# Kernel optimization log

Measured on AMD Instinct MI355X. Metric: run time of the kernel, lower is better.

Reference implementation:

```python
import jax, jax.numpy as jnp
import numpy as np

B, D, H, NB = 4096, 2048, 2048, 4
BIN, BOUT = D // NB, H // NB
EPS = 1e-5


def _block_linear(x, W, b):
    # x: [B, nb*bin], W: [nb, bin, bout], b: [nb, bout] -> [B, nb*bout]
    xr = x.reshape(x.shape[0], NB, BIN)
    y = jnp.einsum('bni,nio->bno', xr, W) + b
    return y.reshape(x.shape[0], NB * BOUT)


def setup_inputs() -> dict:
    key = jax.random.key(0)
    ks = jax.random.split(key, 24)
    sW = 1.0 / np.sqrt(BIN)
    sR = 1.0 / np.sqrt(BOUT)
    inp = {
        'x': jax.random.normal(ks[0], (B, D), jnp.float32),
        'h_prev': jax.random.normal(ks[1], (B, H), jnp.float32),
        'c_prev': jax.random.normal(ks[2], (B, H), jnp.float32),
        'ln_g': jnp.ones((D,), jnp.float32),
        'ln_b': jnp.zeros((D,), jnp.float32),
        'conv_w': jax.random.normal(ks[3], (3,), jnp.float32) * 0.5,
        'conv_b': jnp.zeros((), jnp.float32),
    }
    names = ['Wz', 'Wi', 'Wf', 'Wo']
    for j, n in enumerate(names):
        inp[n] = jax.random.normal(ks[4 + j], (NB, BIN, BOUT), jnp.float32) * sW
        inp['b' + n[1]] = jax.random.normal(ks[8 + j], (NB, BOUT), jnp.float32) * sW
    rnames = ['Rz', 'Ri', 'Rf', 'Ro']
    for j, n in enumerate(rnames):
        inp[n] = jax.random.normal(ks[12 + j], (NB, BOUT, BOUT), jnp.float32) * sR
        inp['rb' + n[1]] = jax.random.normal(ks[16 + j], (NB, BOUT), jnp.float32) * sR
    return inp


def reference(x, h_prev, c_prev, ln_g, ln_b, conv_w, conv_b,
              Wz, bz, Wi, bi, Wf, bf, Wo, bo,
              Rz, rbz, Ri, rbi, Rf, rbf, Ro, rbo):
    # LayerNorm over the feature dim
    mu = jnp.mean(x, axis=-1, keepdims=True)
    var = jnp.mean((x - mu) ** 2, axis=-1, keepdims=True)
    x_norm = (x - mu) * jax.lax.rsqrt(var + EPS) * ln_g + ln_b

    # Causal conv1d (kernel 3) along the feature axis, then SiLU
    xp = jnp.pad(x_norm, ((0, 0), (2, 0)))  # left-pad 2 -> causal
    xc = conv_w[0] * xp[:, :D] + conv_w[1] * xp[:, 1:D + 1] + conv_w[2] * xp[:, 2:D + 2] + conv_b
    x_conv = jax.nn.silu(xc)

    z = jnp.tanh(_block_linear(x, Wz, bz) + _block_linear(h_prev, Rz, rbz))
    i = jax.nn.sigmoid(_block_linear(x_conv, Wi, bi) + _block_linear(h_prev, Ri, rbi))
    f = jax.nn.sigmoid(_block_linear(x_conv, Wf, bf) + _block_linear(h_prev, Rf, rbf))
    o = jax.nn.sigmoid(_block_linear(x, Wo, bo) + _block_linear(h_prev, Ro, rbo))

    c_t = f * c_prev + i * z
    h_t = o * jnp.tanh(c_t)
    return (h_t, c_t)
```

## Files before the change

kernel.cpp:

```cpp
#include <hip/hip_runtime.h>
#include <hip/hip_bf16.h>
#include <math.h>

#define BB 4096
#define DD 2048
#define HH 2048

typedef __bf16 bf16x8 __attribute__((ext_vector_type(8)));
typedef float f32x16 __attribute__((ext_vector_type(16)));

__device__ __forceinline__ void async16(const void* g, void* l) {
  __builtin_amdgcn_global_load_lds(
      (const __attribute__((address_space(1))) unsigned int*)g,
      (__attribute__((address_space(3))) unsigned int*)l,
      16, 0, 0);
}

__device__ __forceinline__ float sigmoidf_(float x) {
  return 1.0f / (1.0f + __expf(-x));
}

__global__ void prep_bias(const float* __restrict__ bz, const float* __restrict__ bi,
                          const float* __restrict__ bf, const float* __restrict__ bo,
                          const float* __restrict__ rbz, const float* __restrict__ rbi,
                          const float* __restrict__ rbf, const float* __restrict__ rbo,
                          float* __restrict__ bias) {
  int i = blockIdx.x * 256 + threadIdx.x;
  if (i < 2048) {
    bias[0 * 2048 + i] = bz[i] + rbz[i];
    bias[1 * 2048 + i] = bi[i] + rbi[i];
    bias[2 * 2048 + i] = bf[i] + rbf[i];
    bias[3 * 2048 + i] = bo[i] + rbo[i];
  }
}

__global__ void prep_w(const float* __restrict__ Wz, const float* __restrict__ Wi,
                       const float* __restrict__ Wf, const float* __restrict__ Wo,
                       const float* __restrict__ Rz, const float* __restrict__ Ri,
                       const float* __restrict__ Rf, const float* __restrict__ Ro,
                       __hip_bfloat16* __restrict__ WT) {
  int jt = blockIdx.x;
  int ktt = blockIdx.y;
  int gn = blockIdx.z;
  int g = gn >> 2, nn = gn & 3;
  int ktg0 = ktt * 32;
  const float* src;
  if (ktg0 < 512) src = (g == 0 ? Wz : g == 1 ? Wi : g == 2 ? Wf : Wo);
  else            src = (g == 0 ? Rz : g == 1 ? Ri : g == 2 ? Rf : Ro);
  int ks0 = ktg0 & 511;
  int j0 = jt * 32;
  __shared__ float tile[32][33];
  int tx = threadIdx.x, ty = threadIdx.y;
#pragma unroll
  for (int r = 0; r < 4; r++) {
    int kk = ty + r * 8;
    tile[kk][tx] = src[((size_t)nn * 512 + ks0 + kk) * 512 + j0 + tx];
  }
  __syncthreads();
#pragma unroll
  for (int r = 0; r < 4; r++) {
    int jj = ty + r * 8;
    WT[((size_t)gn * 512 + j0 + jj) * 1024 + ktg0 + tx] = __float2bfloat16(tile[tx][jj]);
  }
}

__global__ __launch_bounds__(256) void prep_act(
    const float* __restrict__ x, const float* __restrict__ h,
    const float* __restrict__ lg, const float* __restrict__ lb,
    const float* __restrict__ cw, const float* __restrict__ cb,
    __hip_bfloat16* __restrict__ xb, __hip_bfloat16* __restrict__ xcb,
    __hip_bfloat16* __restrict__ hb) {
  int row = blockIdx.x;
  int t = threadIdx.x;
  __shared__ float xn[2048];
  __shared__ float red[8];
  const float* xr = x + (size_t)row * 2048;
  const float* hr = h + (size_t)row * 2048;
  float4 v0 = ((const float4*)xr)[t * 2];
  float4 v1 = ((const float4*)xr)[t * 2 + 1];
  float vv[8] = {v0.x, v0.y, v0.z, v0.w, v1.x, v1.y, v1.z, v1.w};
  float s = 0.f, s2 = 0.f;
#pragma unroll
  for (int e = 0; e < 8; e++) { s += vv[e]; s2 += vv[e] * vv[e]; }
#pragma unroll
  for (int off = 32; off > 0; off >>= 1) {
    s += __shfl_down(s, off);
    s2 += __shfl_down(s2, off);
  }
  int w = t >> 6, l = t & 63;
  if (l == 0) { red[w] = s; red[4 + w] = s2; }
  __syncthreads();
  float mu = (red[0] + red[1] + red[2] + red[3]) * (1.0f / 2048.0f);
  float var = (red[4] + red[5] + red[6] + red[7]) * (1.0f / 2048.0f) - mu * mu;
  float rs = rsqrtf(var + 1e-5f);

  float4 h0 = ((const float4*)hr)[t * 2];
  float4 h1 = ((const float4*)hr)[t * 2 + 1];
  float hh[8] = {h0.x, h0.y, h0.z, h0.w, h1.x, h1.y, h1.z, h1.w};
  int j0 = t * 8;
#pragma unroll
  for (int e = 0; e < 8; e++) {
    int j = j0 + e;
    xn[j] = (vv[e] - mu) * rs * lg[j] + lb[j];
    xb[(size_t)row * 2048 + j] = __float2bfloat16(vv[e]);
    hb[(size_t)row * 2048 + j] = __float2bfloat16(hh[e]);
  }
  __syncthreads();
  float w0 = cw[0], w1 = cw[1], w2 = cw[2], bbv = cb[0];
#pragma unroll
  for (int e = 0; e < 8; e++) {
    int j = j0 + e;
    float a0 = (j >= 2) ? xn[j - 2] : 0.f;
    float a1 = (j >= 1) ? xn[j - 1] : 0.f;
    float xc = w0 * a0 + w1 * a1 + w2 * xn[j] + bbv;
    float sc = xc * sigmoidf_(xc);
    xcb[(size_t)row * 2048 + j] = __float2bfloat16(sc);
  }
}

__global__ __launch_bounds__(256, 2) void gemm_fused(
    const __hip_bfloat16* __restrict__ xb, const __hip_bfloat16* __restrict__ xcb,
    const __hip_bfloat16* __restrict__ hb, const __hip_bfloat16* __restrict__ WT,
    const float* __restrict__ bias, const float* __restrict__ c_prev,
    float* __restrict__ out) {
  __shared__ alignas(16) __hip_bfloat16 As1[64 * 32];
  __shared__ alignas(16) __hip_bfloat16 As2[64 * 32];
  __shared__ alignas(16) __hip_bfloat16 Bs[4][64 * 32];

  const int m0 = blockIdx.x * 64;
  const int j0 = blockIdx.y * 64;
  const int n = blockIdx.z;
  const int t = threadIdx.x;
  const int w = t >> 6, l = t & 63;
  const int wr = w >> 1, wc = w & 1;

  f32x16 accZ = {}, accI = {}, accF = {}, accO = {};

  const size_t a_goff = (size_t)(m0 + (t >> 2)) * 2048 + (size_t)n * 512 + (size_t)((t & 3) * 8);
  char* As1w = (char*)As1 + w * 1024;
  char* As2w = (char*)As2 + w * 1024;
  const size_t b_gbase = ((size_t)(w * 4 + n) * 512 + j0) * 1024;
  char* Bw = (char*)Bs[w];

  const int a_eoff = (wr * 32 + (l & 31)) * 32 + ((l >> 5) * 8);
  const int b_eoff = (wc * 32 + (l & 31)) * 32 + ((l >> 5) * 8);

  for (int ks = 0; ks < 32; ++ks) {
    const int kt = ks * 32;
    const bool ph0 = (kt < 512);
    const __hip_bfloat16* a1 = ph0 ? xb : hb;
    const __hip_bfloat16* a2 = ph0 ? xcb : hb;
    const int kk = kt & 511;

    __syncthreads();
    async16(a1 + a_goff + kk, As1w);
    async16(a2 + a_goff + kk, As2w);
#pragma unroll
    for (int q = 0; q < 4; ++q) {
      int idx = q * 64 + l;
      async16(WT + b_gbase + (size_t)(idx >> 2) * 1024 + kt + (idx & 3) * 8,
              Bw + q * 1024);
    }
    __syncthreads();

#pragma unroll
    for (int kh = 0; kh < 2; ++kh) {
      bf16x8 a1f = *(const bf16x8*)(As1 + a_eoff + kh * 16);
      bf16x8 a2f = *(const bf16x8*)(As2 + a_eoff + kh * 16);
      bf16x8 bzf = *(const bf16x8*)(Bs[0] + b_eoff + kh * 16);
      bf16x8 bif = *(const bf16x8*)(Bs[1] + b_eoff + kh * 16);
      bf16x8 bff = *(const bf16x8*)(Bs[2] + b_eoff + kh * 16);
      bf16x8 bof = *(const bf16x8*)(Bs[3] + b_eoff + kh * 16);
      accZ = __builtin_amdgcn_mfma_f32_32x32x16_bf16(a1f, bzf, accZ, 0, 0, 0);
      accI = __builtin_amdgcn_mfma_f32_32x32x16_bf16(a2f, bif, accI, 0, 0, 0);
      accF = __builtin_amdgcn_mfma_f32_32x32x16_bf16(a2f, bff, accF, 0, 0, 0);
      accO = __builtin_amdgcn_mfma_f32_32x32x16_bf16(a1f, bof, accO, 0, 0, 0);
    }
  }

  const int col = n * 512 + j0 + wc * 32 + (l & 31);
  const float bz_ = bias[0 * 2048 + col];
  const float bi_ = bias[1 * 2048 + col];
  const float bf_ = bias[2 * 2048 + col];
  const float bo_ = bias[3 * 2048 + col];
  const size_t HC = (size_t)BB * HH;
#pragma unroll
  for (int r = 0; r < 16; ++r) {
    int row = m0 + wr * 32 + (r & 3) + 8 * (r >> 2) + 4 * (l >> 5);
    float z = tanhf(accZ[r] + bz_);
    float ig = sigmoidf_(accI[r] + bi_);
    float fg = sigmoidf_(accF[r] + bf_);
    float og = sigmoidf_(accO[r] + bo_);
    float cp = c_prev[(size_t)row * 2048 + col];
    float c = fg * cp + ig * z;
    float hv = og * tanhf(c);
    out[(size_t)row * 2048 + col] = hv;
    out[HC + (size_t)row * 2048 + col] = c;
  }
}

extern "C" void kernel_launch(void* const* d_in, const int* in_sizes, int n_in,
                              void* d_out, int out_size, void* d_ws, size_t ws_size,
                              hipStream_t stream) {
  const float* x      = (const float*)d_in[0];
  const float* h_prev = (const float*)d_in[1];
  const float* c_prev = (const float*)d_in[2];
  const float* ln_g   = (const float*)d_in[3];
  const float* ln_b   = (const float*)d_in[4];
  const float* conv_w = (const float*)d_in[5];
  const float* conv_b = (const float*)d_in[6];
  const float* Wz = (const float*)d_in[7];
  const float* bz = (const float*)d_in[8];
  const float* Wi = (const float*)d_in[9];
  const float* bi = (const float*)d_in[10];
  const float* Wf = (const float*)d_in[11];
  const float* bf = (const float*)d_in[12];
  const float* Wo = (const float*)d_in[13];
  const float* bo = (const float*)d_in[14];
  const float* Rz = (const float*)d_in[15];
  const float* rbz = (const float*)d_in[16];
  const float* Ri = (const float*)d_in[17];
  const float* rbi = (const float*)d_in[18];
  const float* Rf = (const float*)d_in[19];
  const float* rbf = (const float*)d_in[20];
  const float* Ro = (const float*)d_in[21];
  const float* rbo = (const float*)d_in[22];
  float* out = (float*)d_out;

  char* ws = (char*)d_ws;
  const size_t SZ = (size_t)BB * DD * sizeof(__hip_bfloat16);
  __hip_bfloat16* xb  = (__hip_bfloat16*)(ws);
  __hip_bfloat16* xcb = (__hip_bfloat16*)(ws + SZ);
  __hip_bfloat16* hb  = (__hip_bfloat16*)(ws + 2 * SZ);
  __hip_bfloat16* WT  = (__hip_bfloat16*)(ws + 3 * SZ);
  float* bias         = (float*)(ws + 4 * SZ);

  prep_bias<<<8, 256, 0, stream>>>(bz, bi, bf, bo, rbz, rbi, rbf, rbo, bias);
  prep_w<<<dim3(16, 32, 16), dim3(32, 8), 0, stream>>>(Wz, Wi, Wf, Wo, Rz, Ri, Rf, Ro, WT);
  prep_act<<<BB, 256, 0, stream>>>(x, h_prev, ln_g, ln_b, conv_w, conv_b, xb, xcb, hb);
  gemm_fused<<<dim3(BB / 64, 512 / 64, 4), 256, 0, stream>>>(xb, xcb, hb, WT, bias, c_prev, out);
}
```

Measured before the change: 357.9 us.

## Enlarge GEMM tile to 128 rows, split gates across wave pairs, vectorize bf16 stores

The fused gate GEMM now uses a 128x64 tile per block with 16x16x32 MFMAs. Each wave pair owns two gates (z/o or i/f) over 64 rows, so each wave keeps 32 small accumulators instead of four 32x32 ones. The z and o activations are exchanged through LDS as bf16 so the other pair can compute the cell update. Phase 1 skips the redundant second A-tile load, and the prep kernel writes bf16 with 16-byte vector stores. This raises register pressure, drops the 2-block occupancy hint, and rounds z/o to bf16 before the cell update, which slightly changes precision.

New measurement: 498.3 us. +39.2%, slower.

```diff
diff --git a/kernel.cpp b/kernel.cpp
--- a/kernel.cpp
+++ b/kernel.cpp
@@ -7,7 +7,7 @@
 #define HH 2048
 
 typedef __bf16 bf16x8 __attribute__((ext_vector_type(8)));
-typedef float f32x16 __attribute__((ext_vector_type(16)));
+typedef float f32x4 __attribute__((ext_vector_type(4)));
 
 __device__ __forceinline__ void async16(const void* g, void* l) {
   __builtin_amdgcn_global_load_lds(
@@ -18,6 +18,13 @@
 
 __device__ __forceinline__ float sigmoidf_(float x) {
   return 1.0f / (1.0f + __expf(-x));
+}
+
+__device__ __forceinline__ void store_bf8(__hip_bfloat16* dst, const float* v) {
+  union { __hip_bfloat16 b[8]; uint4 u; } p;
+#pragma unroll
+  for (int e = 0; e < 8; e++) p.b[e] = __float2bfloat16(v[e]);
+  *(uint4*)dst = p.u;
 }
 
 __global__ void prep_bias(const float* __restrict__ bz, const float* __restrict__ bi,
@@ -102,100 +109,138 @@
   for (int e = 0; e < 8; e++) {
     int j = j0 + e;
     xn[j] = (vv[e] - mu) * rs * lg[j] + lb[j];
-    xb[(size_t)row * 2048 + j] = __float2bfloat16(vv[e]);
-    hb[(size_t)row * 2048 + j] = __float2bfloat16(hh[e]);
-  }
+  }
+  store_bf8(xb + (size_t)row * 2048 + j0, vv);
+  store_bf8(hb + (size_t)row * 2048 + j0, hh);
   __syncthreads();
   float w0 = cw[0], w1 = cw[1], w2 = cw[2], bbv = cb[0];
+  float sc[8];
 #pragma unroll
   for (int e = 0; e < 8; e++) {
     int j = j0 + e;
     float a0 = (j >= 2) ? xn[j - 2] : 0.f;
     float a1 = (j >= 1) ? xn[j - 1] : 0.f;
     float xc = w0 * a0 + w1 * a1 + w2 * xn[j] + bbv;
-    float sc = xc * sigmoidf_(xc);
-    xcb[(size_t)row * 2048 + j] = __float2bfloat16(sc);
-  }
-}
-
-__global__ __launch_bounds__(256, 2) void gemm_fused(
+    sc[e] = xc * sigmoidf_(xc);
+  }
+  store_bf8(xcb + (size_t)row * 2048 + j0, sc);
+}
+
+__global__ __launch_bounds__(256) void gemm_fused(
     const __hip_bfloat16* __restrict__ xb, const __hip_bfloat16* __restrict__ xcb,
     const __hip_bfloat16* __restrict__ hb, const __hip_bfloat16* __restrict__ WT,
     const float* __restrict__ bias, const float* __restrict__ c_prev,
     float* __restrict__ out) {
-  __shared__ alignas(16) __hip_bfloat16 As1[64 * 32];
-  __shared__ alignas(16) __hip_bfloat16 As2[64 * 32];
-  __shared__ alignas(16) __hip_bfloat16 Bs[4][64 * 32];
-
-  const int m0 = blockIdx.x * 64;
+  __shared__ __attribute__((aligned(16))) char smem[34816];
+  __hip_bfloat16* As1 = (__hip_bfloat16*)smem;
+  __hip_bfloat16* As2 = (__hip_bfloat16*)(smem + 8192);
+  __hip_bfloat16* Bs  = (__hip_bfloat16*)(smem + 16384);
+  __hip_bfloat16* zo  = (__hip_bfloat16*)smem;
+
+  const int m0 = blockIdx.x * 128;
   const int j0 = blockIdx.y * 64;
-  const int n = blockIdx.z;
+  const int n  = blockIdx.z;
   const int t = threadIdx.x;
   const int w = t >> 6, l = t & 63;
-  const int wr = w >> 1, wc = w & 1;
-
-  f32x16 accZ = {}, accI = {}, accF = {}, accO = {};
-
-  const size_t a_goff = (size_t)(m0 + (t >> 2)) * 2048 + (size_t)n * 512 + (size_t)((t & 3) * 8);
-  char* As1w = (char*)As1 + w * 1024;
-  char* As2w = (char*)As2 + w * 1024;
-  const size_t b_gbase = ((size_t)(w * 4 + n) * 512 + j0) * 1024;
-  char* Bw = (char*)Bs[w];
-
-  const int a_eoff = (wr * 32 + (l & 31)) * 32 + ((l >> 5) * 8);
-  const int b_eoff = (wc * 32 + (l & 31)) * 32 + ((l >> 5) * 8);
+  const int pair = w >> 1;
+  const int mhalf = w & 1;
+  const int g0 = pair ? 1 : 0;
+  const int g1 = pair ? 2 : 3;
+
+  f32x4 acc[4][4][2] = {};
+
+  const unsigned aoff1 = (unsigned)(m0 + (t >> 2)) * 2048 + (unsigned)n * 512 + (t & 3) * 8;
+  const unsigned aoff2 = aoff1 + 64u * 2048u;
+  char* As1d = (char*)As1 + w * 1024;
+  char* As2d = (char*)As2 + w * 1024;
+  const unsigned bbase = ((unsigned)(w * 4 + n) * 512 + j0 + (l >> 2)) * 1024 + (l & 3) * 8;
+  char* Bd = (char*)Bs + w * 4096;
+
+  const int lj = l & 15;
+  const int lk = (l >> 4) * 8;
 
   for (int ks = 0; ks < 32; ++ks) {
     const int kt = ks * 32;
     const bool ph0 = (kt < 512);
+    const int kk = kt & 511;
     const __hip_bfloat16* a1 = ph0 ? xb : hb;
-    const __hip_bfloat16* a2 = ph0 ? xcb : hb;
-    const int kk = kt & 511;
 
     __syncthreads();
-    async16(a1 + a_goff + kk, As1w);
-    async16(a2 + a_goff + kk, As2w);
-#pragma unroll
-    for (int q = 0; q < 4; ++q) {
-      int idx = q * 64 + l;
-      async16(WT + b_gbase + (size_t)(idx >> 2) * 1024 + kt + (idx & 3) * 8,
-              Bw + q * 1024);
-    }
+    async16(a1 + aoff1 + kk, As1d);
+    async16(a1 + aoff2 + kk, As1d + 4096);
+    if (ph0) {
+      async16(xcb + aoff1 + kk, As2d);
+      async16(xcb + aoff2 + kk, As2d + 4096);
+    }
+#pragma unroll
+    for (int q = 0; q < 4; ++q)
+      async16(WT + bbase + (unsigned)q * 16u * 1024u + kt, Bd + q * 1024);
     __syncthreads();
 
-#pragma unroll
-    for (int kh = 0; kh < 2; ++kh) {
-      bf16x8 a1f = *(const bf16x8*)(As1 + a_eoff + kh * 16);
-      bf16x8 a2f = *(const bf16x8*)(As2 + a_eoff + kh * 16);
-      bf16x8 bzf = *(const bf16x8*)(Bs[0] + b_eoff + kh * 16);
-      bf16x8 bif = *(const bf16x8*)(Bs[1] + b_eoff + kh * 16);
-      bf16x8 bff = *(const bf16x8*)(Bs[2] + b_eoff + kh * 16);
-      bf16x8 bof = *(const bf16x8*)(Bs[3] + b_eoff + kh * 16);
-      accZ = __builtin_amdgcn_mfma_f32_32x32x16_bf16(a1f, bzf, accZ, 0, 0, 0);
-      accI = __builtin_amdgcn_mfma_f32_32x32x16_bf16(a2f, bif, accI, 0, 0, 0);
-      accF = __builtin_amdgcn_mfma_f32_32x32x16_bf16(a2f, bff, accF, 0, 0, 0);
-      accO = __builtin_amdgcn_mfma_f32_32x32x16_bf16(a1f, bof, accO, 0, 0, 0);
-    }
-  }
-
-  const int col = n * 512 + j0 + wc * 32 + (l & 31);
-  const float bz_ = bias[0 * 2048 + col];
-  const float bi_ = bias[1 * 2048 + col];
-  const float bf_ = bias[2 * 2048 + col];
-  const float bo_ = bias[3 * 2048 + col];
-  const size_t HC = (size_t)BB * HH;
-#pragma unroll
-  for (int r = 0; r < 16; ++r) {
-    int row = m0 + wr * 32 + (r & 3) + 8 * (r >> 2) + 4 * (l >> 5);
-    float z = tanhf(accZ[r] + bz_);
-    float ig = sigmoidf_(accI[r] + bi_);
-    float fg = sigmoidf_(accF[r] + bf_);
-    float og = sigmoidf_(accO[r] + bo_);
-    float cp = c_prev[(size_t)row * 2048 + col];
-    float c = fg * cp + ig * z;
-    float hv = og * tanhf(c);
-    out[(size_t)row * 2048 + col] = hv;
-    out[HC + (size_t)row * 2048 + col] = c;
+    const __hip_bfloat16* Ab = (ph0 ? (pair ? As2 : As1) : As1) + mhalf * 64 * 32;
+    bf16x8 af[4];
+#pragma unroll
+    for (int s = 0; s < 4; ++s)
+      af[s] = *(const bf16x8*)(Ab + (s * 16 + lj) * 32 + lk);
+#pragma unroll
+    for (int sj = 0; sj < 4; ++sj) {
+      bf16x8 b0 = *(const bf16x8*)(Bs + g0 * 2048 + (sj * 16 + lj) * 32 + lk);
+      bf16x8 b1 = *(const bf16x8*)(Bs + g1 * 2048 + (sj * 16 + lj) * 32 + lk);
+#pragma unroll
+      for (int s = 0; s < 4; ++s) {
+        acc[s][sj][0] = __builtin_amdgcn_mfma_f32_16x16x32_bf16(af[s], b0, acc[s][sj][0], 0, 0, 0);
+        acc[s][sj][1] = __builtin_amdgcn_mfma_f32_16x16x32_bf16(af[s], b1, acc[s][sj][1], 0, 0, 0);
+      }
+    }
+  }
+
+  const int r0 = (l >> 4) * 4;
+  const int colbase = n * 512 + j0;
+  __syncthreads();
+  if (pair == 0) {
+#pragma unroll
+    for (int sj = 0; sj < 4; ++sj) {
+      const int jc = sj * 16 + lj;
+      const float bz_ = bias[0 * 2048 + colbase + jc];
+      const float bo_ = bias[3 * 2048 + colbase + jc];
+#pragma unroll
+      for (int s = 0; s < 4; ++s) {
+#pragma unroll
+        for (int r = 0; r < 4; ++r) {
+          const int lm = mhalf * 64 + s * 16 + r0 + r;
+          zo[(0 * 128 + lm) * 68 + jc] = __float2bfloat16(tanhf(acc[s][sj][0][r] + bz_));
+          zo[(1 * 128 + lm) * 68 + jc] = __float2bfloat16(sigmoidf_(acc[s][sj][1][r] + bo_));
+        }
+      }
+    }
+  }
+  __syncthreads();
+  if (pair == 1) {
+    const size_t HC = (size_t)BB * HH;
+#pragma unroll
+    for (int sj = 0; sj < 4; ++sj) {
+      const int jc = sj * 16 + lj;
+      const int col = colbase + jc;
+      const float bi_ = bias[1 * 2048 + col];
+      const float bf_ = bias[2 * 2048 + col];
+#pragma unroll
+      for (int s = 0; s < 4; ++s) {
+#pragma unroll
+        for (int r = 0; r < 4; ++r) {
+          const int lm = mhalf * 64 + s * 16 + r0 + r;
+          const int row = m0 + lm;
+          const float z  = __bfloat162float(zo[(0 * 128 + lm) * 68 + jc]);
+          const float og = __bfloat162float(zo[(1 * 128 + lm) * 68 + jc]);
+          const float ig = sigmoidf_(acc[s][sj][0][r] + bi_);
+          const float fg = sigmoidf_(acc[s][sj][1][r] + bf_);
+          const float cp = c_prev[(size_t)row * 2048 + col];
+          const float c = fg * cp + ig * z;
+          const float hv = og * tanhf(c);
+          out[(size_t)row * 2048 + col] = hv;
+          out[HC + (size_t)row * 2048 + col] = c;
+        }
+      }
+    }
   }
 }
 
@@ -238,5 +283,5 @@
   prep_bias<<<8, 256, 0, stream>>>(bz, bi, bf, bo, rbz, rbi, rbf, rbo, bias);
   prep_w<<<dim3(16, 32, 16), dim3(32, 8), 0, stream>>>(Wz, Wi, Wf, Wo, Rz, Ri, Rf, Ro, WT);
   prep_act<<<BB, 256, 0, stream>>>(x, h_prev, ln_g, ln_b, conv_w, conv_b, xb, xcb, hb);
-  gemm_fused<<<dim3(BB / 64, 512 / 64, 4), 256, 0, stream>>>(xb, xcb, hb, WT, bias, c_prev, out);
-}
+  gemm_fused<<<dim3(BB / 128, 512 / 64, 4), 256, 0, stream>>>(xb, xcb, hb, WT, bias, c_prev, out);
+}
```
